# Kernel optimization log

Measured on AMD Instinct MI355X. Metric: run time of the kernel, lower is better.

The kernel has to match this reference:

```python
import jax, jax.numpy as jnp
import numpy as np

K = 8192
D = 256


def setup_inputs() -> dict:
    key = jax.random.key(0)
    k1, k2 = jax.random.split(key)
    z_e_x = jax.random.normal(k1, (32, 32, 32, D), dtype=jnp.float32)
    # matches torch init: uniform(-1/K, 1/K)
    codebook = jax.random.uniform(k2, (K, D), dtype=jnp.float32,
                                  minval=-1.0 / K, maxval=1.0 / K)
    return {"z_e_x": z_e_x, "codebook": codebook}


def reference(z_e_x, codebook):
    # vq(): nearest-neighbor codebook indices under squared L2 distance.
    flat = z_e_x.reshape(-1, z_e_x.shape[-1])            # [N, D]
    # ||z - e||^2 = ||z||^2 - 2 z.e + ||e||^2 ; ||z||^2 constant over argmin
    dots = flat @ codebook.T                              # [N, K]
    cb_sq = jnp.sum(codebook * codebook, axis=-1)         # [K]
    dist = cb_sq[None, :] - 2.0 * dots                    # [N, K]
    indices = jnp.argmin(dist, axis=-1)                   # [N] int
    return indices.reshape(z_e_x.shape[:-1])              # latent index grid
```

## Files before the change

kernel.cpp:

```cpp
#include <hip/hip_runtime.h>
#include <hip/hip_fp16.h>


#define N_Q   32768
#define K_CB  8192
#define D_DIM 256

typedef _Float16 half8 __attribute__((ext_vector_type(8)));
typedef _Float16 half4 __attribute__((ext_vector_type(4)));
typedef float    f32x4 __attribute__((ext_vector_type(4)));

__device__ __forceinline__ void gl_lds16(const _Float16* g, _Float16* l) {
  __builtin_amdgcn_global_load_lds(
      (const __attribute__((address_space(1))) unsigned int*)g,
      (__attribute__((address_space(3))) unsigned int*)l, 16, 0, 0);
}

__global__ void vq_prep_z(const float* __restrict__ z,
                          _Float16* __restrict__ zh, _Float16* __restrict__ zl) {
  int i = blockIdx.x * 256 + threadIdx.x;
  float4 v = ((const float4*)z)[i];
  float xs[4] = {v.x * 16.0f, v.y * 16.0f, v.z * 16.0f, v.w * 16.0f};
  half4 h, l;
#pragma unroll
  for (int j = 0; j < 4; ++j) {
    _Float16 hj = (_Float16)xs[j];
    h[j] = hj;
    l[j] = (_Float16)(xs[j] - (float)hj);
  }
  ((half4*)zh)[i] = h;
  ((half4*)zl)[i] = l;
}

__global__ void vq_prep_cb(const float* __restrict__ cb,
                           _Float16* __restrict__ eh, _Float16* __restrict__ el,
                           float* __restrict__ cbs) {
  int w = threadIdx.x >> 6, lane = threadIdx.x & 63;
  int code = blockIdx.x * 4 + w;
  float4 v = ((const float4*)cb)[code * 64 + lane];
  float ss = v.x * v.x + v.y * v.y + v.z * v.z + v.w * v.w;
  float xs[4] = {v.x * 32768.0f, v.y * 32768.0f, v.z * 32768.0f, v.w * 32768.0f};
  half4 h, l;
#pragma unroll
  for (int j = 0; j < 4; ++j) {
    _Float16 hj = (_Float16)xs[j];
    h[j] = hj;
    l[j] = (_Float16)(xs[j] - (float)hj);
  }
  ((half4*)eh)[code * 64 + lane] = h;
  ((half4*)el)[code * 64 + lane] = l;
#pragma unroll
  for (int off = 1; off < 64; off <<= 1) ss += __shfl_xor(ss, off);
  if (lane == 0) cbs[code] = ss * 524288.0f;
}

__global__ __launch_bounds__(256, 2)
void vq_main(const _Float16* __restrict__ zh, const _Float16* __restrict__ zl,
             const _Float16* __restrict__ eh, const _Float16* __restrict__ el,
             const float* __restrict__ cbs,
             unsigned long long* __restrict__ partials) {
  __shared__ __align__(16) _Float16 Ah[8192], Al[8192], Bh[8192], Bl[8192];
  __shared__ float    redD[2][128];
  __shared__ unsigned redC[2][128];

  const int tid  = threadIdx.x;
  const int lane = tid & 63;
  const int w    = tid >> 6;
  const int q    = lane & 15;
  const int quad = lane >> 4;
  const int wrow = (w >> 1) * 64;
  const int wcol = (w & 1) * 64;

  const int qt    = blockIdx.x >> 1;
  const int split = blockIdx.x & 1;
  const int q0    = qt * 128;
  const int c0    = split * 4096;

  int offA[4][2], offB[4][2];
#pragma unroll
  for (int mt = 0; mt < 4; ++mt) {
    int ra = wrow + mt * 16 + q;
    int rb = wcol + mt * 16 + q;
#pragma unroll
    for (int k2 = 0; k2 < 2; ++k2) {
      int gb = k2 * 4 + quad;
      offA[mt][k2] = ra * 64 + ((gb ^ (ra & 7)) << 3);
      offB[mt][k2] = rb * 64 + ((gb ^ (rb & 7)) << 3);
    }
  }

  float    rd[16];
  unsigned rc[16];
#pragma unroll
  for (int i = 0; i < 16; ++i) { rd[i] = 3.0e38f; rc[i] = 0u; }

  for (int ct = 0; ct < 32; ++ct) {
    const int crow0 = c0 + ct * 128;
    f32x4 acc[4][4];
#pragma unroll
    for (int mt = 0; mt < 4; ++mt)
#pragma unroll
      for (int nt = 0; nt < 4; ++nt)
        acc[mt][nt] = (f32x4){0.f, 0.f, 0.f, 0.f};

    for (int kk = 0; kk < 4; ++kk) {
      const int kcol = kk * 64;
      __syncthreads();
#pragma unroll
      for (int c = 0; c < 4; ++c) {
        int bi   = (w * 4 + c) * 64 + lane;
        int row  = bi >> 3;
        int gb   = (bi & 7) ^ (row & 7);
        int goff = row * 256 + kcol + gb * 8;
        int ldst = (w * 4 + c) * 512;
        gl_lds16(zh + (size_t)q0 * 256 + goff,    &Ah[ldst]);
        gl_lds16(zl + (size_t)q0 * 256 + goff,    &Al[ldst]);
        gl_lds16(eh + (size_t)crow0 * 256 + goff, &Bh[ldst]);
        gl_lds16(el + (size_t)crow0 * 256 + goff, &Bl[ldst]);
      }
      __syncthreads();

#pragma unroll
      for (int k2 = 0; k2 < 2; ++k2) {
        half8 ahf[4], alf[4], bhf[4], blf[4];
#pragma unroll
        for (int i = 0; i < 4; ++i) {
          ahf[i] = *(const half8*)&Ah[offA[i][k2]];
          alf[i] = *(const half8*)&Al[offA[i][k2]];
          bhf[i] = *(const half8*)&Bh[offB[i][k2]];
          blf[i] = *(const half8*)&Bl[offB[i][k2]];
        }
#pragma unroll
        for (int mt = 0; mt < 4; ++mt)
#pragma unroll
          for (int nt = 0; nt < 4; ++nt) {
            acc[mt][nt] = __builtin_amdgcn_mfma_f32_16x16x32_f16(ahf[mt], bhf[nt], acc[mt][nt], 0, 0, 0);
            acc[mt][nt] = __builtin_amdgcn_mfma_f32_16x16x32_f16(ahf[mt], blf[nt], acc[mt][nt], 0, 0, 0);
            acc[mt][nt] = __builtin_amdgcn_mfma_f32_16x16x32_f16(alf[mt], bhf[nt], acc[mt][nt], 0, 0, 0);
          }
      }
    }

    const int cb0 = crow0 + wcol + q;
    float cbsv[4];
#pragma unroll
    for (int nt = 0; nt < 4; ++nt) cbsv[nt] = cbs[cb0 + nt * 16];
#pragma unroll
    for (int mt = 0; mt < 4; ++mt)
#pragma unroll
      for (int r = 0; r < 4; ++r) {
        float d = fmaf(-2.0f, acc[mt][0][r], cbsv[0]);
        unsigned cidx = (unsigned)cb0;
#pragma unroll
        for (int nt = 1; nt < 4; ++nt) {
          float dn = fmaf(-2.0f, acc[mt][nt][r], cbsv[nt]);
          if (dn < d) { d = dn; cidx = (unsigned)(cb0 + nt * 16); }
        }
        int ri = mt * 4 + r;
        if (d < rd[ri]) { rd[ri] = d; rc[ri] = cidx; }
      }
  }

#pragma unroll
  for (int ri = 0; ri < 16; ++ri) {
    float d = rd[ri]; unsigned cidx = rc[ri];
#pragma unroll
    for (int off = 1; off < 16; off <<= 1) {
      float od = __shfl_xor(d, off);
      unsigned oc = __shfl_xor(cidx, off);
      if (od < d || (od == d && oc < cidx)) { d = od; cidx = oc; }
    }
    if (q == 0) {
      int row = wrow + (ri >> 2) * 16 + quad * 4 + (ri & 3);
      redD[w & 1][row] = d;
      redC[w & 1][row] = cidx;
    }
  }
  __syncthreads();
  if (tid < 128) {
    float d0 = redD[0][tid]; unsigned cc0 = redC[0][tid];
    float d1 = redD[1][tid]; unsigned cc1 = redC[1][tid];
    if (d1 < d0 || (d1 == d0 && cc1 < cc0)) { d0 = d1; cc0 = cc1; }
    unsigned u = __float_as_uint(d0);
    u = (u & 0x80000000u) ? ~u : (u | 0x80000000u);
    partials[(size_t)split * N_Q + q0 + tid] = ((unsigned long long)u << 32) | cc0;
  }
}

__global__ void vq_final(const unsigned long long* __restrict__ partials,
                         int* __restrict__ out) {
  int i = blockIdx.x * 256 + threadIdx.x;
  unsigned long long a = partials[i], b = partials[(size_t)N_Q + i];
  unsigned long long m = (b < a) ? b : a;
  out[i] = (int)(unsigned)(m & 0xffffffffull);
}

extern "C" void kernel_launch(void* const* d_in, const int* in_sizes, int n_in,
                              void* d_out, int out_size, void* d_ws, size_t ws_size,
                              hipStream_t stream) {
  const float* z  = (const float*)d_in[0];
  const float* cb = (const float*)d_in[1];
  char* ws = (char*)d_ws;
  _Float16* zh = (_Float16*)(ws);
  _Float16* zl = (_Float16*)(ws + (size_t)16 * 1024 * 1024);
  _Float16* eh = (_Float16*)(ws + (size_t)32 * 1024 * 1024);
  _Float16* el = (_Float16*)(ws + (size_t)36 * 1024 * 1024);
  float*    cbs = (float*)(ws + (size_t)40 * 1024 * 1024);
  unsigned long long* partials =
      (unsigned long long*)(ws + (size_t)40 * 1024 * 1024 + 65536);

  hipLaunchKernelGGL(vq_prep_z,  dim3(8192), dim3(256), 0, stream, z, zh, zl);
  hipLaunchKernelGGL(vq_prep_cb, dim3(2048), dim3(256), 0, stream, cb, eh, el, cbs);
  hipLaunchKernelGGL(vq_main,    dim3(512),  dim3(256), 0, stream,
                     zh, zl, eh, el, cbs, partials);
  hipLaunchKernelGGL(vq_final,   dim3(128),  dim3(256), 0, stream,
                     partials, (int*)d_out);
}
```

Before: 445.9 us.

## Halve LDS footprint, split codebook four ways, raise occupancy to four blocks

```diff
diff --git a/kernel.cpp b/kernel.cpp
--- a/kernel.cpp
+++ b/kernel.cpp
@@ -54,12 +54,12 @@
   if (lane == 0) cbs[code] = ss * 524288.0f;
 }
 
-__global__ __launch_bounds__(256, 2)
+__global__ __launch_bounds__(256, 4)
 void vq_main(const _Float16* __restrict__ zh, const _Float16* __restrict__ zl,
              const _Float16* __restrict__ eh, const _Float16* __restrict__ el,
              const float* __restrict__ cbs,
              unsigned long long* __restrict__ partials) {
-  __shared__ __align__(16) _Float16 Ah[8192], Al[8192], Bh[8192], Bl[8192];
+  __shared__ __align__(16) _Float16 A[8192], B[8192];
   __shared__ float    redD[2][128];
   __shared__ unsigned redC[2][128];
 
@@ -71,22 +71,20 @@
   const int wrow = (w >> 1) * 64;
   const int wcol = (w & 1) * 64;
 
-  const int qt    = blockIdx.x >> 1;
-  const int split = blockIdx.x & 1;
+  const int qt    = blockIdx.x >> 2;
+  const int split = blockIdx.x & 3;
   const int q0    = qt * 128;
-  const int c0    = split * 4096;
+  const int c0    = split * 2048;
 
   int offA[4][2], offB[4][2];
 #pragma unroll
   for (int mt = 0; mt < 4; ++mt) {
     int ra = wrow + mt * 16 + q;
     int rb = wcol + mt * 16 + q;
-#pragma unroll
-    for (int k2 = 0; k2 < 2; ++k2) {
-      int gb = k2 * 4 + quad;
-      offA[mt][k2] = ra * 64 + ((gb ^ (ra & 7)) << 3);
-      offB[mt][k2] = rb * 64 + ((gb ^ (rb & 7)) << 3);
-    }
+    offA[mt][0] = ra * 64 + (((quad    ) ^ (ra & 7)) << 3);
+    offA[mt][1] = ra * 64 + (((quad + 4) ^ (ra & 7)) << 3);
+    offB[mt][0] = rb * 64 + (((quad    ) ^ (rb & 7)) << 3);
+    offB[mt][1] = rb * 64 + (((quad + 4) ^ (rb & 7)) << 3);
   }
 
   float    rd[16];
@@ -94,7 +92,7 @@
 #pragma unroll
   for (int i = 0; i < 16; ++i) { rd[i] = 3.0e38f; rc[i] = 0u; }
 
-  for (int ct = 0; ct < 32; ++ct) {
+  for (int ct = 0; ct < 16; ++ct) {
     const int crow0 = c0 + ct * 128;
     f32x4 acc[4][4];
 #pragma unroll
@@ -103,42 +101,41 @@
       for (int nt = 0; nt < 4; ++nt)
         acc[mt][nt] = (f32x4){0.f, 0.f, 0.f, 0.f};
 
-    for (int kk = 0; kk < 4; ++kk) {
-      const int kcol = kk * 64;
+    for (int kk = 0; kk < 8; ++kk) {
+      const int kcol = kk * 32;
       __syncthreads();
 #pragma unroll
       for (int c = 0; c < 4; ++c) {
         int bi   = (w * 4 + c) * 64 + lane;
         int row  = bi >> 3;
-        int gb   = (bi & 7) ^ (row & 7);
-        int goff = row * 256 + kcol + gb * 8;
+        int g    = (bi & 7) ^ (row & 7);
+        int ksub = (g & 3) * 8;
+        const _Float16* asrc = (g < 4 ? zh : zl)
+                             + (size_t)(q0 + row) * 256 + kcol + ksub;
+        const _Float16* bsrc = (g < 4 ? eh : el)
+                             + (size_t)(crow0 + row) * 256 + kcol + ksub;
         int ldst = (w * 4 + c) * 512;
-        gl_lds16(zh + (size_t)q0 * 256 + goff,    &Ah[ldst]);
-        gl_lds16(zl + (size_t)q0 * 256 + goff,    &Al[ldst]);
-        gl_lds16(eh + (size_t)crow0 * 256 + goff, &Bh[ldst]);
-        gl_lds16(el + (size_t)crow0 * 256 + goff, &Bl[ldst]);
+        gl_lds16(asrc, &A[ldst]);
+        gl_lds16(bsrc, &B[ldst]);
       }
       __syncthreads();
 
-#pragma unroll
-      for (int k2 = 0; k2 < 2; ++k2) {
-        half8 ahf[4], alf[4], bhf[4], blf[4];
-#pragma unroll
-        for (int i = 0; i < 4; ++i) {
-          ahf[i] = *(const half8*)&Ah[offA[i][k2]];
-          alf[i] = *(const half8*)&Al[offA[i][k2]];
-          bhf[i] = *(const half8*)&Bh[offB[i][k2]];
-          blf[i] = *(const half8*)&Bl[offB[i][k2]];
+      half8 ahf[4], alf[4], bhf[4], blf[4];
+#pragma unroll
+      for (int i = 0; i < 4; ++i) {
+        ahf[i] = *(const half8*)&A[offA[i][0]];
+        alf[i] = *(const half8*)&A[offA[i][1]];
+        bhf[i] = *(const half8*)&B[offB[i][0]];
+        blf[i] = *(const half8*)&B[offB[i][1]];
+      }
+#pragma unroll
+      for (int mt = 0; mt < 4; ++mt)
+#pragma unroll
+        for (int nt = 0; nt < 4; ++nt) {
+          acc[mt][nt] = __builtin_amdgcn_mfma_f32_16x16x32_f16(ahf[mt], bhf[nt], acc[mt][nt], 0, 0, 0);
+          acc[mt][nt] = __builtin_amdgcn_mfma_f32_16x16x32_f16(ahf[mt], blf[nt], acc[mt][nt], 0, 0, 0);
+          acc[mt][nt] = __builtin_amdgcn_mfma_f32_16x16x32_f16(alf[mt], bhf[nt], acc[mt][nt], 0, 0, 0);
         }
-#pragma unroll
-        for (int mt = 0; mt < 4; ++mt)
-#pragma unroll
-          for (int nt = 0; nt < 4; ++nt) {
-            acc[mt][nt] = __builtin_amdgcn_mfma_f32_16x16x32_f16(ahf[mt], bhf[nt], acc[mt][nt], 0, 0, 0);
-            acc[mt][nt] = __builtin_amdgcn_mfma_f32_16x16x32_f16(ahf[mt], blf[nt], acc[mt][nt], 0, 0, 0);
-            acc[mt][nt] = __builtin_amdgcn_mfma_f32_16x16x32_f16(alf[mt], bhf[nt], acc[mt][nt], 0, 0, 0);
-          }
-      }
     }
 
     const int cb0 = crow0 + wcol + q;
@@ -190,8 +187,12 @@
 __global__ void vq_final(const unsigned long long* __restrict__ partials,
                          int* __restrict__ out) {
   int i = blockIdx.x * 256 + threadIdx.x;
-  unsigned long long a = partials[i], b = partials[(size_t)N_Q + i];
-  unsigned long long m = (b < a) ? b : a;
+  unsigned long long m = partials[i];
+#pragma unroll
+  for (int s = 1; s < 4; ++s) {
+    unsigned long long v = partials[(size_t)s * N_Q + i];
+    if (v < m) m = v;
+  }
   out[i] = (int)(unsigned)(m & 0xffffffffull);
 }
 
@@ -211,7 +212,7 @@
 
   hipLaunchKernelGGL(vq_prep_z,  dim3(8192), dim3(256), 0, stream, z, zh, zl);
   hipLaunchKernelGGL(vq_prep_cb, dim3(2048), dim3(256), 0, stream, cb, eh, el, cbs);
-  hipLaunchKernelGGL(vq_main,    dim3(512),  dim3(256), 0, stream,
+  hipLaunchKernelGGL(vq_main,    dim3(1024), dim3(256), 0, stream,
                      zh, zl, eh, el, cbs, partials);
   hipLaunchKernelGGL(vq_final,   dim3(128),  dim3(256), 0, stream,
                      partials, (int*)d_out);
```

Measured after the change: 961.9 us. 116% more time.

## Double-buffer LDS tiles and switch to 32x32x16 MFMA with merged hi/lo staging

Applied to the files above, without the earlier changes.

```diff
diff --git a/kernel.cpp b/kernel.cpp
--- a/kernel.cpp
+++ b/kernel.cpp
@@ -4,11 +4,15 @@
 
 #define N_Q   32768
 #define K_CB  8192
-#define D_DIM 256
+
+#define ZH_OFF 0u
+#define ZL_OFF 8388608u
+#define EH_OFF 16777216u
+#define EL_OFF 18874368u
 
 typedef _Float16 half8 __attribute__((ext_vector_type(8)));
 typedef _Float16 half4 __attribute__((ext_vector_type(4)));
-typedef float    f32x4 __attribute__((ext_vector_type(4)));
+typedef float    f32x16 __attribute__((ext_vector_type(16)));
 
 __device__ __forceinline__ void gl_lds16(const _Float16* g, _Float16* l) {
   __builtin_amdgcn_global_load_lds(
@@ -55,19 +59,16 @@
 }
 
 __global__ __launch_bounds__(256, 2)
-void vq_main(const _Float16* __restrict__ zh, const _Float16* __restrict__ zl,
-             const _Float16* __restrict__ eh, const _Float16* __restrict__ el,
+void vq_main(const _Float16* __restrict__ ws,
              const float* __restrict__ cbs,
              unsigned long long* __restrict__ partials) {
-  __shared__ __align__(16) _Float16 Ah[8192], Al[8192], Bh[8192], Bl[8192];
+  __shared__ __align__(16) _Float16 S[2][16384];
   __shared__ float    redD[2][128];
   __shared__ unsigned redC[2][128];
 
   const int tid  = threadIdx.x;
   const int lane = tid & 63;
   const int w    = tid >> 6;
-  const int q    = lane & 15;
-  const int quad = lane >> 4;
   const int wrow = (w >> 1) * 64;
   const int wcol = (w & 1) * 64;
 
@@ -76,114 +77,156 @@
   const int q0    = qt * 128;
   const int c0    = split * 4096;
 
-  int offA[4][2], offB[4][2];
-#pragma unroll
-  for (int mt = 0; mt < 4; ++mt) {
-    int ra = wrow + mt * 16 + q;
-    int rb = wcol + mt * 16 + q;
-#pragma unroll
-    for (int k2 = 0; k2 < 2; ++k2) {
-      int gb = k2 * 4 + quad;
-      offA[mt][k2] = ra * 64 + ((gb ^ (ra & 7)) << 3);
-      offB[mt][k2] = rb * 64 + ((gb ^ (rb & 7)) << 3);
-    }
-  }
-
-  float    rd[16];
-  unsigned rc[16];
-#pragma unroll
-  for (int i = 0; i < 16; ++i) { rd[i] = 3.0e38f; rc[i] = 0u; }
-
-  for (int ct = 0; ct < 32; ++ct) {
-    const int crow0 = c0 + ct * 128;
-    f32x4 acc[4][4];
-#pragma unroll
-    for (int mt = 0; mt < 4; ++mt)
-#pragma unroll
-      for (int nt = 0; nt < 4; ++nt)
-        acc[mt][nt] = (f32x4){0.f, 0.f, 0.f, 0.f};
-
-    for (int kk = 0; kk < 4; ++kk) {
-      const int kcol = kk * 64;
-      __syncthreads();
+  unsigned srcA[4], srcB[4];
+#pragma unroll
+  for (int c = 0; c < 4; ++c) {
+    int bi = c * 256 + tid;
+    int r  = bi >> 3;
+    int p  = bi & 7;
+    int g  = p ^ (r & 7);
+    int hl = g >> 2;
+    int kb = g & 3;
+    srcA[c] = (hl ? ZL_OFF : ZH_OFF) + (unsigned)(q0 + r) * 256u + kb * 8;
+    srcB[c] = (hl ? EL_OFF : EH_OFF) + (unsigned)(c0 + r) * 256u + kb * 8;
+  }
+
+  int offA[2][2][2], offB[2][2][2];
+#pragma unroll
+  for (int t = 0; t < 2; ++t)
+#pragma unroll
+    for (int kk = 0; kk < 2; ++kk)
+#pragma unroll
+      for (int hl = 0; hl < 2; ++hl) {
+        int g  = hl * 4 + kk * 2 + (lane >> 5);
+        int ra = wrow + t * 32 + (lane & 31);
+        int rb = wcol + t * 32 + (lane & 31);
+        offA[t][kk][hl] = ra * 64 + ((g ^ (ra & 7)) << 3);
+        offB[t][kk][hl] = 8192 + rb * 64 + ((g ^ (rb & 7)) << 3);
+      }
+
+  float    rd[2][16];
+  unsigned rc[2][16];
+#pragma unroll
+  for (int mt = 0; mt < 2; ++mt)
+#pragma unroll
+    for (int r = 0; r < 16; ++r) { rd[mt][r] = 3.0e38f; rc[mt][r] = 0u; }
+
+  f32x16 acc[2][2];
+#pragma unroll
+  for (int mt = 0; mt < 2; ++mt)
+#pragma unroll
+    for (int nt = 0; nt < 2; ++nt)
+#pragma unroll
+      for (int r = 0; r < 16; ++r) acc[mt][nt][r] = 0.0f;
+
+  {
+#pragma unroll
+    for (int c = 0; c < 4; ++c) {
+      gl_lds16(ws + srcA[c], &S[0][c * 2048 + w * 512]);
+      gl_lds16(ws + srcB[c], &S[0][8192 + c * 2048 + w * 512]);
+    }
+  }
+  __syncthreads();
+
+  float cb0v = 0.f, cb1v = 0.f;
+
+  for (int u = 0; u < 256; ++u) {
+    const int kkc = u & 7;
+    const int ct  = u >> 3;
+
+    if (kkc == 0) {
+      int colbase = c0 + ct * 128 + wcol + (lane & 31);
+      cb0v = cbs[colbase];
+      cb1v = cbs[colbase + 32];
+    }
+
+    if (u < 255) {
+      int nu = u + 1;
+      unsigned aoff = (unsigned)(nu & 7) * 32u;
+      unsigned boff = (unsigned)(nu >> 3) * 32768u + aoff;
+      _Float16* dst = S[nu & 1];
 #pragma unroll
       for (int c = 0; c < 4; ++c) {
-        int bi   = (w * 4 + c) * 64 + lane;
-        int row  = bi >> 3;
-        int gb   = (bi & 7) ^ (row & 7);
-        int goff = row * 256 + kcol + gb * 8;
-        int ldst = (w * 4 + c) * 512;
-        gl_lds16(zh + (size_t)q0 * 256 + goff,    &Ah[ldst]);
-        gl_lds16(zl + (size_t)q0 * 256 + goff,    &Al[ldst]);
-        gl_lds16(eh + (size_t)crow0 * 256 + goff, &Bh[ldst]);
-        gl_lds16(el + (size_t)crow0 * 256 + goff, &Bl[ldst]);
-      }
-      __syncthreads();
-
-#pragma unroll
-      for (int k2 = 0; k2 < 2; ++k2) {
-        half8 ahf[4], alf[4], bhf[4], blf[4];
-#pragma unroll
-        for (int i = 0; i < 4; ++i) {
-          ahf[i] = *(const half8*)&Ah[offA[i][k2]];
-          alf[i] = *(const half8*)&Al[offA[i][k2]];
-          bhf[i] = *(const half8*)&Bh[offB[i][k2]];
-          blf[i] = *(const half8*)&Bl[offB[i][k2]];
+        gl_lds16(ws + srcA[c] + aoff, &dst[c * 2048 + w * 512]);
+        gl_lds16(ws + srcB[c] + boff, &dst[8192 + c * 2048 + w * 512]);
+      }
+    }
+
+    {
+      const _Float16* B = S[u & 1];
+      half8 ah[2][2], al[2][2], bh[2][2], bl[2][2];
+#pragma unroll
+      for (int t = 0; t < 2; ++t)
+#pragma unroll
+        for (int kk = 0; kk < 2; ++kk) {
+          ah[t][kk] = *(const half8*)&B[offA[t][kk][0]];
+          al[t][kk] = *(const half8*)&B[offA[t][kk][1]];
+          bh[t][kk] = *(const half8*)&B[offB[t][kk][0]];
+          bl[t][kk] = *(const half8*)&B[offB[t][kk][1]];
         }
 #pragma unroll
-        for (int mt = 0; mt < 4; ++mt)
-#pragma unroll
-          for (int nt = 0; nt < 4; ++nt) {
-            acc[mt][nt] = __builtin_amdgcn_mfma_f32_16x16x32_f16(ahf[mt], bhf[nt], acc[mt][nt], 0, 0, 0);
-            acc[mt][nt] = __builtin_amdgcn_mfma_f32_16x16x32_f16(ahf[mt], blf[nt], acc[mt][nt], 0, 0, 0);
-            acc[mt][nt] = __builtin_amdgcn_mfma_f32_16x16x32_f16(alf[mt], bhf[nt], acc[mt][nt], 0, 0, 0);
+      for (int kk = 0; kk < 2; ++kk)
+#pragma unroll
+        for (int mt = 0; mt < 2; ++mt)
+#pragma unroll
+          for (int nt = 0; nt < 2; ++nt) {
+            acc[mt][nt] = __builtin_amdgcn_mfma_f32_32x32x16_f16(
+                ah[mt][kk], bh[nt][kk], acc[mt][nt], 0, 0, 0);
+            acc[mt][nt] = __builtin_amdgcn_mfma_f32_32x32x16_f16(
+                ah[mt][kk], bl[nt][kk], acc[mt][nt], 0, 0, 0);
+            acc[mt][nt] = __builtin_amdgcn_mfma_f32_32x32x16_f16(
+                al[mt][kk], bh[nt][kk], acc[mt][nt], 0, 0, 0);
           }
-      }
-    }
-
-    const int cb0 = crow0 + wcol + q;
-    float cbsv[4];
-#pragma unroll
-    for (int nt = 0; nt < 4; ++nt) cbsv[nt] = cbs[cb0 + nt * 16];
-#pragma unroll
-    for (int mt = 0; mt < 4; ++mt)
-#pragma unroll
-      for (int r = 0; r < 4; ++r) {
-        float d = fmaf(-2.0f, acc[mt][0][r], cbsv[0]);
-        unsigned cidx = (unsigned)cb0;
-#pragma unroll
-        for (int nt = 1; nt < 4; ++nt) {
-          float dn = fmaf(-2.0f, acc[mt][nt][r], cbsv[nt]);
-          if (dn < d) { d = dn; cidx = (unsigned)(cb0 + nt * 16); }
+    }
+
+    if (kkc == 7) {
+      int colbase = c0 + ct * 128 + wcol + (lane & 31);
+#pragma unroll
+      for (int mt = 0; mt < 2; ++mt)
+#pragma unroll
+        for (int r = 0; r < 16; ++r) {
+          float d0 = fmaf(-2.0f, acc[mt][0][r], cb0v);
+          float d1 = fmaf(-2.0f, acc[mt][1][r], cb1v);
+          float d;
+          unsigned ci;
+          if (d1 < d0) { d = d1; ci = (unsigned)(colbase + 32); }
+          else         { d = d0; ci = (unsigned)colbase; }
+          if (d < rd[mt][r]) { rd[mt][r] = d; rc[mt][r] = ci; }
+          acc[mt][0][r] = 0.0f;
+          acc[mt][1][r] = 0.0f;
         }
-        int ri = mt * 4 + r;
-        if (d < rd[ri]) { rd[ri] = d; rc[ri] = cidx; }
-      }
-  }
-
-#pragma unroll
-  for (int ri = 0; ri < 16; ++ri) {
-    float d = rd[ri]; unsigned cidx = rc[ri];
-#pragma unroll
-    for (int off = 1; off < 16; off <<= 1) {
-      float od = __shfl_xor(d, off);
-      unsigned oc = __shfl_xor(cidx, off);
-      if (od < d || (od == d && oc < cidx)) { d = od; cidx = oc; }
-    }
-    if (q == 0) {
-      int row = wrow + (ri >> 2) * 16 + quad * 4 + (ri & 3);
-      redD[w & 1][row] = d;
-      redC[w & 1][row] = cidx;
-    }
-  }
+    }
+
+    __syncthreads();
+  }
+
+#pragma unroll
+  for (int mt = 0; mt < 2; ++mt)
+#pragma unroll
+    for (int r = 0; r < 16; ++r) {
+      float d = rd[mt][r];
+      unsigned ci = rc[mt][r];
+#pragma unroll
+      for (int off = 1; off < 32; off <<= 1) {
+        float od = __shfl_xor(d, off);
+        unsigned oc = __shfl_xor(ci, off);
+        if (od < d || (od == d && oc < ci)) { d = od; ci = oc; }
+      }
+      if ((lane & 31) == 0) {
+        int row = wrow + mt * 32 + (r & 3) + 8 * (r >> 2) + 4 * (lane >> 5);
+        redD[w & 1][row] = d;
+        redC[w & 1][row] = ci;
+      }
+    }
   __syncthreads();
   if (tid < 128) {
     float d0 = redD[0][tid]; unsigned cc0 = redC[0][tid];
     float d1 = redD[1][tid]; unsigned cc1 = redC[1][tid];
     if (d1 < d0 || (d1 == d0 && cc1 < cc0)) { d0 = d1; cc0 = cc1; }
-    unsigned u = __float_as_uint(d0);
-    u = (u & 0x80000000u) ? ~u : (u | 0x80000000u);
-    partials[(size_t)split * N_Q + q0 + tid] = ((unsigned long long)u << 32) | cc0;
+    unsigned uu = __float_as_uint(d0);
+    uu = (uu & 0x80000000u) ? ~uu : (uu | 0x80000000u);
+    partials[(size_t)split * N_Q + q0 + tid] =
+        ((unsigned long long)uu << 32) | cc0;
   }
 }
 
@@ -212,7 +255,7 @@
   hipLaunchKernelGGL(vq_prep_z,  dim3(8192), dim3(256), 0, stream, z, zh, zl);
   hipLaunchKernelGGL(vq_prep_cb, dim3(2048), dim3(256), 0, stream, cb, eh, el, cbs);
   hipLaunchKernelGGL(vq_main,    dim3(512),  dim3(256), 0, stream,
-                     zh, zl, eh, el, cbs, partials);
+                     (const _Float16*)ws, cbs, partials);
   hipLaunchKernelGGL(vq_final,   dim3(128),  dim3(256), 0, stream,
                      partials, (int*)d_out);
 }
```

Result: slower. 546.8 us (+22.6%).
